# Kernel tuning notes

Measured on AMD Instinct MI355X. Metric: run time of the kernel, lower is better.

The kernel has to match this reference:

```python
import jax, jax.numpy as jnp
import numpy as np

B, S, E, H, D = 2, 2048, 1024, 16, 64


def setup_inputs() -> dict:
    key = jax.random.key(0)
    ks = jax.random.split(key, 6)
    hidden_states = jax.random.normal(ks[0], (B, S, E), dtype=jnp.float32)
    # causal mask over (SeqLen, KeySeqLen): 1 = attend, 0 = blocked
    mask = jnp.tril(jnp.ones((S, S), dtype=jnp.float32))
    W_attn = jax.random.normal(ks[1], (E, 3, H, D), dtype=jnp.float32) * (E ** -0.5)
    b_attn = jnp.zeros((3, H, D), dtype=jnp.float32)
    W_proj = jax.random.normal(ks[2], (H, D, E), dtype=jnp.float32) * (E ** -0.5)
    b_proj = jnp.zeros((E,), dtype=jnp.float32)
    W_v_ff = jax.random.normal(ks[3], (E, E), dtype=jnp.float32) * (E ** -0.5)
    W_v_gate = jax.random.normal(ks[4], (E, E), dtype=jnp.float32) * (E ** -0.5)
    return {
        "hidden_states": hidden_states,
        "mask": mask,
        "layer_idx": 3,
        "W_attn": W_attn,
        "b_attn": b_attn,
        "W_proj": W_proj,
        "b_proj": b_proj,
        "W_v_ff": W_v_ff,
        "W_v_gate": W_v_gate,
    }


def reference(hidden_states, mask, layer_idx, W_attn, b_attn, W_proj, b_proj, W_v_ff, W_v_gate):
    dtype = hidden_states.dtype
    # c_attn: [B,S,E] -> [B,3,S,H,D]
    qkv = jnp.einsum("bse,eqhd->bqshd", hidden_states, W_attn) + b_attn[:, None, :, :]
    q, k, v = qkv[:, 0], qkv[:, 1], qkv[:, 2]  # [B,S,H,D] (k,v use key-seq axis)

    scale = jax.lax.rsqrt(float(D)) / (layer_idx + 1.0)  # scale_by_inverse_layer_idx
    q = q * scale
    # upcast to fp32 for score computation
    q32 = q.astype(jnp.float32)
    k32 = k.astype(jnp.float32)

    # attention scores: [B,H,S,Skv]
    scores = jnp.einsum("bshd,bthd->bhst", q32, k32)
    scores = scores + (1.0 - mask) * -1e9
    attn_weights = jax.nn.softmax(scores, axis=-1).astype(dtype)
    # dropout is identity (inference=True / p=0)

    # gated V FFN applied over the flattened (H,D) == Embed axis of v
    v_flat = v.reshape(B, S, E)
    v_gate = v_flat @ W_v_gate
    v_ff = v_flat @ W_v_ff
    v_gated = (jax.nn.relu(v_gate) * v_ff).reshape(B, S, H, D)

    # weighted sum over KeySeqLen: [B,S,H,D]
    attn_output = jnp.einsum("bhst,bthd->bshd", attn_weights, v_gated)
    # c_proj: [B,S,H,D] -> [B,S,E]
    out = jnp.einsum("bshd,hde->bse", attn_output, W_proj) + b_proj
    return out
```

## Files before the change

### kernel.cpp

```cpp
#include <hip/hip_runtime.h>
#include <hip/hip_bf16.h>
#include <cstdint>
#include <cstddef>

typedef unsigned short u16;
typedef __bf16 bf16x8 __attribute__((ext_vector_type(8)));
typedef float f32x4 __attribute__((ext_vector_type(4)));

#define LOG2E 1.44269504088896340736f

__device__ __forceinline__ uint32_t f2bf2(float lo, float hi) {
  uint32_t r;
  asm("v_cvt_pk_bf16_f32 %0, %1, %2" : "=v"(r) : "v"(lo), "v"(hi));
  return r;
}
__device__ __forceinline__ u16 f2bf(float f) { return (u16)f2bf2(f, f); }

__device__ __forceinline__ void gload16(const u16* g, u16* l) {
  __builtin_amdgcn_global_load_lds(
      (const __attribute__((address_space(1))) void*)g,
      (__attribute__((address_space(3))) void*)l, 16, 0, 0);
}

__global__ __launch_bounds__(256) void transpose_bf16_kernel(
    const float* __restrict__ src, u16* __restrict__ dst, int ld, int c0) {
  __shared__ u16 tile[64][65];
  const int r0 = blockIdx.x * 64, cl0 = blockIdx.y * 64;
  const int tid = threadIdx.x;
#pragma unroll
  for (int i = 0; i < 16; ++i) {
    int idx = i * 256 + tid;
    int r = idx >> 6, c = idx & 63;
    tile[c][r] = f2bf(src[(size_t)(r0 + r) * ld + c0 + cl0 + c]);
  }
  __syncthreads();
#pragma unroll
  for (int i = 0; i < 16; ++i) {
    int idx = i * 256 + tid;
    int c = idx >> 6, r = idx & 63;
    dst[(size_t)(cl0 + c) * 1024 + r0 + r] = tile[c][r];
  }
}

__global__ __launch_bounds__(256) void prep3_kernel(
    const float* __restrict__ Wa, const float* __restrict__ Wg,
    const float* __restrict__ Wf,
    u16* __restrict__ dv, u16* __restrict__ dg, u16* __restrict__ df) {
  __shared__ u16 tile[64][65];
  const int z = blockIdx.z;
  const float* src = (z == 0) ? Wa : (z == 1) ? Wg : Wf;
  u16* dst = (z == 0) ? dv : (z == 1) ? dg : df;
  const int ld = (z == 0) ? 3072 : 1024;
  const int c0 = (z == 0) ? 2048 : 0;
  const int r0 = blockIdx.x * 64, cl0 = blockIdx.y * 64;
  const int tid = threadIdx.x;
#pragma unroll
  for (int i = 0; i < 16; ++i) {
    int idx = i * 256 + tid;
    int r = idx >> 6, c = idx & 63;
    tile[c][r] = f2bf(src[(size_t)(r0 + r) * ld + c0 + cl0 + c]);
  }
  __syncthreads();
#pragma unroll
  for (int i = 0; i < 16; ++i) {
    int idx = i * 256 + tid;
    int c = idx >> 6, r = idx & 63;
    dst[(size_t)(cl0 + c) * 1024 + r0 + r] = tile[c][r];
  }
}

template <int EPI>
__global__ __launch_bounds__(256) void gemm_hA(
    const float* __restrict__ A,
    const u16* __restrict__ Bt,
    u16* __restrict__ O0, u16* __restrict__ O1,
    const float* __restrict__ bias,
    const int* __restrict__ layer_idx) {
  __shared__ u16 lds_a[2][64 * 40];
  __shared__ u16 lds_b[2][128 * 32];
  const int tid = threadIdx.x;
  const int wid = tid >> 6, lane = tid & 63;
  const int lrow = lane & 15, lgrp = lane >> 4;
  const int brow = blockIdx.y * 64;
  const int bcol = blockIdx.x * 128;
  const int wr = wid >> 1, wc = wid & 1;

  f32x4 acc[2][4] = {};

  const int wchunk0 = wid, wchunk1 = 4 + wid;
  const int cB0 = wchunk0 * 64 + lane, cB1 = wchunk1 * 64 + lane;
  const int rB0 = cB0 >> 2, col8B0 = (cB0 & 3) << 3;
  const int rB1 = cB1 >> 2, col8B1 = (cB1 & 3) << 3;

  gload16(Bt + (size_t)(bcol + rB0) * 1024 + col8B0, lds_b[0] + wchunk0 * 512);
  gload16(Bt + (size_t)(bcol + rB1) * 1024 + col8B1, lds_b[0] + wchunk1 * 512);
  {
    float4 v[2];
#pragma unroll
    for (int j = 0; j < 2; ++j) {
      int idx = j * 256 + tid;
      int m = idx >> 3, k4 = (idx & 7) << 2;
      v[j] = *(const float4*)(A + (size_t)(brow + m) * 1024 + k4);
    }
#pragma unroll
    for (int j = 0; j < 2; ++j) {
      int idx = j * 256 + tid;
      int m = idx >> 3, k4 = (idx & 7) << 2;
      uint2 w;
      w.x = f2bf2(v[j].x, v[j].y);
      w.y = f2bf2(v[j].z, v[j].w);
      *(uint2*)(lds_a[0] + m * 40 + k4) = w;
    }
  }

  for (int k0 = 0; k0 < 1024; k0 += 32) {
    const int bi = (k0 >> 5) & 1;
    __syncthreads();
    bf16x8 af[2], bfr[4];
#pragma unroll
    for (int mi = 0; mi < 2; ++mi)
      af[mi] = *(const bf16x8*)(lds_a[bi] + (wr * 32 + mi * 16 + lrow) * 40 + lgrp * 8);
#pragma unroll
    for (int nj = 0; nj < 4; ++nj)
      bfr[nj] = *(const bf16x8*)(lds_b[bi] + (wc * 64 + nj * 16 + lrow) * 32 + lgrp * 8);

    float4 v[2];
    if (k0 < 992) {
      const int kn = k0 + 32;
      gload16(Bt + (size_t)(bcol + rB0) * 1024 + kn + col8B0, lds_b[bi ^ 1] + wchunk0 * 512);
      gload16(Bt + (size_t)(bcol + rB1) * 1024 + kn + col8B1, lds_b[bi ^ 1] + wchunk1 * 512);
#pragma unroll
      for (int j = 0; j < 2; ++j) {
        int idx = j * 256 + tid;
        int m = idx >> 3, k4 = (idx & 7) << 2;
        v[j] = *(const float4*)(A + (size_t)(brow + m) * 1024 + kn + k4);
      }
    }

#pragma unroll
    for (int mi = 0; mi < 2; ++mi)
#pragma unroll
      for (int nj = 0; nj < 4; ++nj)
        acc[mi][nj] = __builtin_amdgcn_mfma_f32_16x16x32_bf16(af[mi], bfr[nj], acc[mi][nj], 0, 0, 0);

    if (k0 < 992) {
#pragma unroll
      for (int j = 0; j < 2; ++j) {
        int idx = j * 256 + tid;
        int m = idx >> 3, k4 = (idx & 7) << 2;
        uint2 w;
        w.x = f2bf2(v[j].x, v[j].y);
        w.y = f2bf2(v[j].z, v[j].w);
        *(uint2*)(lds_a[bi ^ 1] + m * 40 + k4) = w;
      }
    }
  }

  float scale = 1.0f;
  if (EPI == 0) scale = 0.125f * LOG2E / (1.0f + (float)(*layer_idx));

#pragma unroll
  for (int mi = 0; mi < 2; ++mi) {
#pragma unroll
    for (int nj = 0; nj < 4; ++nj) {
#pragma unroll
      for (int r = 0; r < 4; ++r) {
        int row = brow + wr * 32 + mi * 16 + lgrp * 4 + r;
        int col = bcol + wc * 64 + nj * 16 + lrow;
        float vv = acc[mi][nj][r] + bias[col];
        if (EPI == 0) {
          if (col < 1024) {
            O0[(size_t)row * 1024 + col] = f2bf(vv * scale);
          } else {
            O1[(size_t)row * 1024 + (col - 1024)] = f2bf(vv);
          }
        } else {
          size_t oidx = (size_t)(row >> 11) * 4194304 + (size_t)(row & 2047) * 1024 + col;
          O0[oidx] = f2bf(vv);
        }
      }
    }
  }
}

__global__ __launch_bounds__(256) void gemm_gate(
    const u16* __restrict__ A,
    const u16* __restrict__ Bg, const u16* __restrict__ Bf,
    u16* __restrict__ VgT) {
  __shared__ u16 lds_a[2][64 * 32];
  __shared__ u16 lds_g[2][128 * 32];
  __shared__ u16 lds_f[2][128 * 32];
  const int tid = threadIdx.x;
  const int wid = tid >> 6, lane = tid & 63;
  const int lrow = lane & 15, lgrp = lane >> 4;
  const int browg = blockIdx.y * 64;
  const int batch = browg >> 11;
  const int brow = browg & 2047;
  const u16* Ab = A + (size_t)batch * 4194304;
  u16* VgTb = VgT + (size_t)batch * 4194304;
  const int bcol = blockIdx.x * 128;
  const int wr = wid >> 1, wc = wid & 1;

  f32x4 accg[2][4] = {};
  f32x4 accf[2][4] = {};

  const int wchunk0 = wid, wchunk1 = 4 + wid;
  const int cA = wchunk0 * 64 + lane;
  const int rA = cA >> 2, col8A = (cA & 3) << 3;
  const int cB0 = wchunk0 * 64 + lane, cB1 = wchunk1 * 64 + lane;
  const int rB0 = cB0 >> 2, col8B0 = (cB0 & 3) << 3;
  const int rB1 = cB1 >> 2, col8B1 = (cB1 & 3) << 3;

  auto stage = [&](int k0, int bi) {
    gload16(Ab + (size_t)(brow + rA) * 1024 + k0 + col8A, lds_a[bi] + wchunk0 * 512);
    gload16(Bg + (size_t)(bcol + rB0) * 1024 + k0 + col8B0, lds_g[bi] + wchunk0 * 512);
    gload16(Bg + (size_t)(bcol + rB1) * 1024 + k0 + col8B1, lds_g[bi] + wchunk1 * 512);
    gload16(Bf + (size_t)(bcol + rB0) * 1024 + k0 + col8B0, lds_f[bi] + wchunk0 * 512);
    gload16(Bf + (size_t)(bcol + rB1) * 1024 + k0 + col8B1, lds_f[bi] + wchunk1 * 512);
  };

  stage(0, 0);
  for (int k0 = 0; k0 < 1024; k0 += 32) {
    const int bi = (k0 >> 5) & 1;
    __syncthreads();
    bf16x8 af[2], bg[4], bff[4];
#pragma unroll
    for (int mi = 0; mi < 2; ++mi)
      af[mi] = *(const bf16x8*)(lds_a[bi] + (wr * 32 + mi * 16 + lrow) * 32 + lgrp * 8);
#pragma unroll
    for (int nj = 0; nj < 4; ++nj) {
      bg[nj]  = *(const bf16x8*)(lds_g[bi] + (wc * 64 + nj * 16 + lrow) * 32 + lgrp * 8);
      bff[nj] = *(const bf16x8*)(lds_f[bi] + (wc * 64 + nj * 16 + lrow) * 32 + lgrp * 8);
    }
    if (k0 < 992) stage(k0 + 32, bi ^ 1);
#pragma unroll
    for (int mi = 0; mi < 2; ++mi)
#pragma unroll
      for (int nj = 0; nj < 4; ++nj) {
        accg[mi][nj] = __builtin_amdgcn_mfma_f32_16x16x32_bf16(af[mi], bg[nj],  accg[mi][nj], 0, 0, 0);
        accf[mi][nj] = __builtin_amdgcn_mfma_f32_16x16x32_bf16(af[mi], bff[nj], accf[mi][nj], 0, 0, 0);
      }
  }

#pragma unroll
  for (int mi = 0; mi < 2; ++mi) {
#pragma unroll
    for (int nj = 0; nj < 4; ++nj) {
      int row0 = brow + wr * 32 + mi * 16 + lgrp * 4;
      int n = bcol + wc * 64 + nj * 16 + lrow;
      uint2 w;
      w.x = f2bf2(fmaxf(accg[mi][nj][0], 0.f) * accf[mi][nj][0],
                  fmaxf(accg[mi][nj][1], 0.f) * accf[mi][nj][1]);
      w.y = f2bf2(fmaxf(accg[mi][nj][2], 0.f) * accf[mi][nj][2],
                  fmaxf(accg[mi][nj][3], 0.f) * accf[mi][nj][3]);
      *(uint2*)(VgTb + (size_t)n * 2048 + row0) = w;
    }
  }
}

__global__ __launch_bounds__(256) void gemm_projf(
    const u16* __restrict__ A,
    const float* __restrict__ Wp,
    float* __restrict__ Cout,
    const float* __restrict__ bias) {
  __shared__ u16 lds_a[2][64 * 32];
  __shared__ u16 lds_bt[2][64 * 40];
  const int tid = threadIdx.x;
  const int wid = tid >> 6, lane = tid & 63;
  const int lrow = lane & 15, lgrp = lane >> 4;
  const int brow = blockIdx.y * 64;
  const int bcol = blockIdx.x * 64;
  const int wr = wid >> 1, wc = wid & 1;

  f32x4 acc[2][2] = {};

  const int cA = wid * 64 + lane;
  const int rA = cA >> 2, col8A = (cA & 3) << 3;
  const int ng = tid & 15, kp = tid >> 4;
  const int n4 = ng << 2, kk = kp << 1;
  const int kc = kk >> 3, klo = kk & 7;

  auto stageB = [&](int k0, int bi) {
    float4 va = *(const float4*)(Wp + (size_t)(k0 + kk) * 1024 + bcol + n4);
    float4 vb = *(const float4*)(Wp + (size_t)(k0 + kk + 1) * 1024 + bcol + n4);
    const float a4[4] = {va.x, va.y, va.z, va.w};
    const float b4[4] = {vb.x, vb.y, vb.z, vb.w};
#pragma unroll
    for (int i = 0; i < 4; ++i) {
      int row = n4 + i;
      int sw = (kc ^ ((row >> 2) & 3)) << 3;
      u16* p = lds_bt[bi] + row * 40 + sw + klo;
      *(uint32_t*)p = f2bf2(a4[i], b4[i]);
    }
  };

  gload16(A + (size_t)(brow + rA) * 1024 + col8A, lds_a[0] + wid * 512);
  stageB(0, 0);

  for (int k0 = 0; k0 < 1024; k0 += 32) {
    const int bi = (k0 >> 5) & 1;
    __syncthreads();
    bf16x8 af[2], bfr[2];
#pragma unroll
    for (int mi = 0; mi < 2; ++mi)
      af[mi] = *(const bf16x8*)(lds_a[bi] + (wr * 32 + mi * 16 + lrow) * 32 + lgrp * 8);
#pragma unroll
    for (int nj = 0; nj < 2; ++nj) {
      int rowb = wc * 32 + nj * 16 + lrow;
      bfr[nj] = *(const bf16x8*)(lds_bt[bi] + rowb * 40 + ((lgrp ^ ((rowb >> 2) & 3)) << 3));
    }

    if (k0 < 992) {
      const int kn = k0 + 32;
      gload16(A + (size_t)(brow + rA) * 1024 + kn + col8A, lds_a[bi ^ 1] + wid * 512);
      stageB(kn, bi ^ 1);
    }

#pragma unroll
    for (int mi = 0; mi < 2; ++mi)
#pragma unroll
      for (int nj = 0; nj < 2; ++nj)
        acc[mi][nj] = __builtin_amdgcn_mfma_f32_16x16x32_bf16(af[mi], bfr[nj], acc[mi][nj], 0, 0, 0);
  }

#pragma unroll
  for (int mi = 0; mi < 2; ++mi)
#pragma unroll
    for (int nj = 0; nj < 2; ++nj)
#pragma unroll
      for (int r = 0; r < 4; ++r) {
        int row = brow + wr * 32 + mi * 16 + lgrp * 4 + r;
        int col = bcol + wc * 32 + nj * 16 + lrow;
        Cout[(size_t)row * 1024 + col] = acc[mi][nj][r] + bias[col];
      }
}

__global__ __launch_bounds__(256) void attn_kernel(
    const u16* Qb, const u16* __restrict__ Kb,
    const u16* __restrict__ VgTb, u16* AO) {
  __shared__ u16 lds_k[128 * 64];
  __shared__ u16 lds_v[64 * 128];
  __shared__ u16 lds_p[4][16 * 128];
  const int tid = threadIdx.x, wid = tid >> 6, lane = tid & 63;
  const int lrow = lane & 15, lgrp = lane >> 4;
  const int f = blockIdx.x;
  const int h = f & 15;
  const int idx = f >> 4;
  const int qt = (idx < 16) ? idx : 47 - idx;
  const int nt = (qt >> 1) + 1;

  bf16x8 qf[2];
  {
    const u16* qp = Qb + (size_t)(qt * 64 + wid * 16 + lrow) * 1024 + h * 64 + lgrp * 8;
    qf[0] = *(const bf16x8*)(qp);
    qf[1] = *(const bf16x8*)(qp + 32);
  }

  int krow[4], kch[4], vrow[4], vch[4];
#pragma unroll
  for (int i = 0; i < 4; ++i) {
    int c = i * 256 + tid;
    krow[i] = c >> 3; kch[i] = c & 7;
    vrow[i] = c >> 4; vch[i] = c & 15;
  }
  bf16x8 kreg[4], vreg[4];

  auto stage_load = [&](int t) {
#pragma unroll
    for (int i = 0; i < 4; ++i) {
      kreg[i] = *(const bf16x8*)(Kb + (size_t)(t * 128 + krow[i]) * 1024 + h * 64 + kch[i] * 8);
      vreg[i] = *(const bf16x8*)(VgTb + (size_t)(h * 64 + vrow[i]) * 2048 + t * 128 + vch[i] * 8);
    }
  };
  auto stage_write = [&]() {
#pragma unroll
    for (int i = 0; i < 4; ++i) {
      *(bf16x8*)(lds_k + krow[i] * 64 + ((kch[i] ^ (krow[i] & 7)) << 3)) = kreg[i];
      *(bf16x8*)(lds_v + vrow[i] * 128 + ((vch[i] ^ (vrow[i] & 7)) << 3)) = vreg[i];
    }
  };

  stage_load(0);
  stage_write();
  __syncthreads();

  f32x4 oacc[4] = {};
  float lsum[4] = {0.f, 0.f, 0.f, 0.f};
  u16* pw = lds_p[wid];

  for (int t = 0; t < nt; ++t) {
    if (t + 1 < nt) stage_load(t + 1);

    f32x4 sacc[8] = {};
#pragma unroll
    for (int ks = 0; ks < 2; ++ks)
#pragma unroll
      for (int nj = 0; nj < 8; ++nj) {
        bf16x8 kf = *(const bf16x8*)(lds_k + (nj * 16 + lrow) * 64 + (((ks * 4 + lgrp) ^ (lrow & 7)) << 3));
        sacc[nj] = __builtin_amdgcn_mfma_f32_16x16x32_bf16(qf[ks], kf, sacc[nj], 0, 0, 0);
      }

    const bool last = (t == nt - 1);
#pragma unroll
    for (int nj = 0; nj < 8; ++nj) {
#pragma unroll
      for (int r = 0; r < 4; ++r) {
        const int srow = qt * 64 + wid * 16 + lgrp * 4 + r;
        float p;
        if (last && (t * 128 + nj * 16 + lrow > srow)) {
          p = 0.f;
        } else {
          p = exp2f(sacc[nj][r]);
        }
        lsum[r] += p;
        const int prow = lgrp * 4 + r;
        const int pch = (nj * 2 + (lrow >> 3)) ^ (prow & 7);
        pw[prow * 128 + (pch << 3) + (lrow & 7)] = f2bf(p);
      }
    }

#pragma unroll
    for (int ks = 0; ks < 4; ++ks) {
      bf16x8 pf = *(const bf16x8*)(pw + lrow * 128 + (((ks * 4 + lgrp) ^ (lrow & 7)) << 3));
#pragma unroll
      for (int nj = 0; nj < 4; ++nj) {
        bf16x8 vf = *(const bf16x8*)(lds_v + (nj * 16 + lrow) * 128 + (((ks * 4 + lgrp) ^ (lrow & 7)) << 3));
        oacc[nj] = __builtin_amdgcn_mfma_f32_16x16x32_bf16(pf, vf, oacc[nj], 0, 0, 0);
      }
    }

    if (t + 1 < nt) {
      __syncthreads();
      stage_write();
      __syncthreads();
    }
  }

#pragma unroll
  for (int r = 0; r < 4; ++r) {
#pragma unroll
    for (int off = 1; off < 16; off <<= 1) lsum[r] += __shfl_xor(lsum[r], off);
    lsum[r] = 1.0f / lsum[r];
  }

#pragma unroll
  for (int nj = 0; nj < 4; ++nj) {
#pragma unroll
    for (int r = 0; r < 4; ++r) {
      const int srow = qt * 64 + wid * 16 + lgrp * 4 + r;
      AO[(size_t)srow * 1024 + h * 64 + nj * 16 + lrow] = f2bf(oacc[nj][r] * lsum[r]);
    }
  }
}

extern "C" void kernel_launch(void* const* d_in, const int* in_sizes, int n_in,
                              void* d_out, int out_size, void* d_ws, size_t ws_size,
                              hipStream_t stream) {
  const float* hidden    = (const float*)d_in[0];
  const int*   layer_idx = (const int*)d_in[2];
  const float* W_attn    = (const float*)d_in[3];
  const float* b_attn    = (const float*)d_in[4];
  const float* W_proj    = (const float*)d_in[5];
  const float* b_proj    = (const float*)d_in[6];
  const float* W_v_ff    = (const float*)d_in[7];
  const float* W_v_gate  = (const float*)d_in[8];

  const size_t MB = 1ull << 20;
  char* ob = (char*)d_out;
  u16* QA = (u16*)(ob);
  u16* QB = (u16*)(ob + 4 * MB);
  u16* QC = (u16*)(ob + 8 * MB);
  u16* QD = (u16*)(ob + 12 * MB);
  u16* WS  = (u16*)d_ws;
  u16* WfT = WS + 1024 * 1024;

  const float* hid0 = hidden;
  const float* hid1 = hidden + (size_t)2048 * 1024;

  prep3_kernel<<<dim3(16, 16, 3), 256, 0, stream>>>(W_attn, W_v_gate, W_v_ff, QD, WS, WfT);
  gemm_hA<1><<<dim3(8, 64), 256, 0, stream>>>(hidden, QD, QA, nullptr, b_attn + 2048, nullptr);
  gemm_gate<<<dim3(8, 64), 256, 0, stream>>>(QA, WS, WfT, QB);
  transpose_bf16_kernel<<<dim3(16, 32), 256, 0, stream>>>(W_attn, QC, 3072, 0);
  gemm_hA<0><<<dim3(16, 32), 256, 0, stream>>>(hid0, QC, WS, QA, b_attn, layer_idx);
  attn_kernel<<<512, 256, 0, stream>>>(WS, QA, QB, WS);
  gemm_hA<0><<<dim3(16, 32), 256, 0, stream>>>(hid1, QC, QA, QB, b_attn, layer_idx);
  attn_kernel<<<512, 256, 0, stream>>>(QA, QB, QD, QA);
  gemm_projf<<<dim3(16, 32), 256, 0, stream>>>(QA, W_proj, (float*)d_out + (size_t)2048 * 1024, b_proj);
  gemm_projf<<<dim3(16, 32), 256, 0, stream>>>(WS, W_proj, (float*)d_out, b_proj);
}
```

Measured before the change: 233.7 us.

## Load K and gated-V fragments directly from global memory, drop LDS staging

The attention kernel stops staging K and V tiles through shared memory with block-wide barriers. Each wave now loads its MFMA operand fragments straight from global memory into registers. The block-to-(head, query tile) mapping is also reordered so that paired light and heavy causal tiles and heads are grouped, which is meant to improve L2 locality. This removes the __syncthreads and LDS traffic, but each of the four waves now fetches K and V redundantly, which raises global/L2 traffic and register pressure.

```diff
diff --git a/kernel.cpp b/kernel.cpp
--- a/kernel.cpp
+++ b/kernel.cpp
@@ -338,15 +338,14 @@
 __global__ __launch_bounds__(256) void attn_kernel(
     const u16* Qb, const u16* __restrict__ Kb,
     const u16* __restrict__ VgTb, u16* AO) {
-  __shared__ u16 lds_k[128 * 64];
-  __shared__ u16 lds_v[64 * 128];
   __shared__ u16 lds_p[4][16 * 128];
   const int tid = threadIdx.x, wid = tid >> 6, lane = tid & 63;
   const int lrow = lane & 15, lgrp = lane >> 4;
-  const int f = blockIdx.x;
-  const int h = f & 15;
-  const int idx = f >> 4;
-  const int qt = (idx < 16) ? idx : 47 - idx;
+  const int b = blockIdx.x;
+  const int slot = b >> 3;
+  const int hl = slot >> 5, g = slot & 31;
+  const int h = ((b & 7) << 1) | hl;
+  const int qt = hl ? (31 - g) : g;
   const int nt = (qt >> 1) + 1;
 
   bf16x8 qf[2];
@@ -356,49 +355,34 @@
     qf[1] = *(const bf16x8*)(qp + 32);
   }
 
-  int krow[4], kch[4], vrow[4], vch[4];
-#pragma unroll
-  for (int i = 0; i < 4; ++i) {
-    int c = i * 256 + tid;
-    krow[i] = c >> 3; kch[i] = c & 7;
-    vrow[i] = c >> 4; vch[i] = c & 15;
-  }
-  bf16x8 kreg[4], vreg[4];
-
-  auto stage_load = [&](int t) {
-#pragma unroll
-    for (int i = 0; i < 4; ++i) {
-      kreg[i] = *(const bf16x8*)(Kb + (size_t)(t * 128 + krow[i]) * 1024 + h * 64 + kch[i] * 8);
-      vreg[i] = *(const bf16x8*)(VgTb + (size_t)(h * 64 + vrow[i]) * 2048 + t * 128 + vch[i] * 8);
-    }
-  };
-  auto stage_write = [&]() {
-#pragma unroll
-    for (int i = 0; i < 4; ++i) {
-      *(bf16x8*)(lds_k + krow[i] * 64 + ((kch[i] ^ (krow[i] & 7)) << 3)) = kreg[i];
-      *(bf16x8*)(lds_v + vrow[i] * 128 + ((vch[i] ^ (vrow[i] & 7)) << 3)) = vreg[i];
-    }
-  };
-
-  stage_load(0);
-  stage_write();
-  __syncthreads();
+  const u16* Kh = Kb + h * 64;
+  const u16* Vh = VgTb + (size_t)(h * 64) * 2048;
 
   f32x4 oacc[4] = {};
   float lsum[4] = {0.f, 0.f, 0.f, 0.f};
   u16* pw = lds_p[wid];
 
   for (int t = 0; t < nt; ++t) {
-    if (t + 1 < nt) stage_load(t + 1);
+    bf16x8 kf[2][8];
+#pragma unroll
+    for (int ks = 0; ks < 2; ++ks)
+#pragma unroll
+      for (int nj = 0; nj < 8; ++nj)
+        kf[ks][nj] = *(const bf16x8*)(Kh + (size_t)(t * 128 + nj * 16 + lrow) * 1024 + (ks * 4 + lgrp) * 8);
 
     f32x4 sacc[8] = {};
 #pragma unroll
     for (int ks = 0; ks < 2; ++ks)
 #pragma unroll
-      for (int nj = 0; nj < 8; ++nj) {
-        bf16x8 kf = *(const bf16x8*)(lds_k + (nj * 16 + lrow) * 64 + (((ks * 4 + lgrp) ^ (lrow & 7)) << 3));
-        sacc[nj] = __builtin_amdgcn_mfma_f32_16x16x32_bf16(qf[ks], kf, sacc[nj], 0, 0, 0);
-      }
+      for (int nj = 0; nj < 8; ++nj)
+        sacc[nj] = __builtin_amdgcn_mfma_f32_16x16x32_bf16(qf[ks], kf[ks][nj], sacc[nj], 0, 0, 0);
+
+    bf16x8 vf[4][4];
+#pragma unroll
+    for (int ks = 0; ks < 4; ++ks)
+#pragma unroll
+      for (int nj = 0; nj < 4; ++nj)
+        vf[ks][nj] = *(const bf16x8*)(Vh + (size_t)(nj * 16 + lrow) * 2048 + t * 128 + (ks * 4 + lgrp) * 8);
 
     const bool last = (t == nt - 1);
 #pragma unroll
@@ -423,16 +407,8 @@
     for (int ks = 0; ks < 4; ++ks) {
       bf16x8 pf = *(const bf16x8*)(pw + lrow * 128 + (((ks * 4 + lgrp) ^ (lrow & 7)) << 3));
 #pragma unroll
-      for (int nj = 0; nj < 4; ++nj) {
-        bf16x8 vf = *(const bf16x8*)(lds_v + (nj * 16 + lrow) * 128 + (((ks * 4 + lgrp) ^ (lrow & 7)) << 3));
-        oacc[nj] = __builtin_amdgcn_mfma_f32_16x16x32_bf16(pf, vf, oacc[nj], 0, 0, 0);
-      }
-    }
-
-    if (t + 1 < nt) {
-      __syncthreads();
-      stage_write();
-      __syncthreads();
+      for (int nj = 0; nj < 4; ++nj)
+        oacc[nj] = __builtin_amdgcn_mfma_f32_16x16x32_bf16(pf, vf[ks][nj], oacc[nj], 0, 0, 0);
     }
   }
 
```

After: 286.5 us. 22.6% more time.
